# Kernel tuning notes

Measured on AMD Instinct MI355X. Metric: run time of the kernel, lower is better.

Reference implementation:

```python
import jax, jax.numpy as jnp
import numpy as np
from jax import lax

DIM = 64
E = int(DIM * 1.2)  # 76
E4 = E * 4          # 304
P = 8               # patch size
B, H, W = 2, 256, 256
THR = 1e-10


def setup_inputs() -> dict:
    key = jax.random.key(0)
    ks = jax.random.split(key, 5)
    x = jax.random.normal(ks[0], (B, DIM, H, W), dtype=jnp.float32)
    w_hidden = jax.random.normal(ks[1], (E4, DIM), dtype=jnp.float32) * 0.05
    w_dw = jax.random.normal(ks[2], (E4, 1, 3, 3), dtype=jnp.float32) * 0.2
    w_proj = jax.random.normal(ks[3], (DIM, 3 * E), dtype=jnp.float32) * 0.05
    fft_param = jnp.ones((E, 1, 1, P, P // 2 + 1), dtype=jnp.float32)
    ln1_w = jnp.ones((E,), jnp.float32); ln1_b = jnp.zeros((E,), jnp.float32)
    ln2_w = jnp.ones((E,), jnp.float32); ln2_b = jnp.zeros((E,), jnp.float32)
    ln3_w = jnp.ones((E,), jnp.float32); ln3_b = jnp.zeros((E,), jnp.float32)
    return dict(x=x, w_hidden=w_hidden, w_dw=w_dw, w_proj=w_proj,
                fft_param=fft_param, ln1_w=ln1_w, ln1_b=ln1_b,
                ln2_w=ln2_w, ln2_b=ln2_b, ln3_w=ln3_w, ln3_b=ln3_b)


def _replace_denormals(z, thr=THR):
    r, i = z.real, z.imag
    r = jnp.where((r < thr) & (r > -thr), thr, r)
    i = jnp.where((i < thr) & (i > -thr), thr, i)
    return lax.complex(r, i)


def _patch(t):  # b c H W -> b c h w P P
    b, c, h, w = t.shape
    return t.reshape(b, c, h // P, P, w // P, P).transpose(0, 1, 2, 4, 3, 5)


def _unpatch(t):  # b c h w P P -> b c H W
    b, c, h, w, p1, p2 = t.shape
    return t.transpose(0, 1, 2, 4, 3, 5).reshape(b, c, h * p1, w * p2)


def _layernorm(t, w, b):  # normalize over channel axis (axis=1), biased var
    mu = jnp.mean(t, axis=1, keepdims=True)
    var = jnp.mean((t - mu) ** 2, axis=1, keepdims=True)
    return (t - mu) / jnp.sqrt(var + 1e-5) * w[None, :, None, None] + b[None, :, None, None]


def reference(x, w_hidden, w_dw, w_proj, fft_param,
              ln1_w, ln1_b, ln2_w, ln2_b, ln3_w, ln3_b):
    hidden = jnp.einsum('bchw,oc->bohw', x, w_hidden)  # 1x1 conv
    hdw = lax.conv_general_dilated(
        hidden, w_dw, window_strides=(1, 1), padding='SAME',
        dimension_numbers=('NCHW', 'OIHW', 'NCHW'), feature_group_count=E4)
    q, k, v, v_value = jnp.split(hdw, 4, axis=1)

    qf = jnp.fft.rfft2(_patch(q))
    kf = jnp.fft.rfft2(_patch(k))
    vf = jnp.fft.rfft2(_patch(v)) * fft_param  # broadcast [E,1,1,P,P//2+1]
    vf = _replace_denormals(vf)

    qk = _replace_denormals(qf * kf)
    qka = jnp.abs(qk)
    v_a = jnp.abs(vf)
    v_p = jnp.arctan2(vf.imag, vf.real)

    qf = _replace_denormals(qf)
    kf = _replace_denormals(kf)
    qkp = jnp.arctan2(qf.imag, qf.real) - jnp.arctan2(kf.imag, kf.real)

    out1 = jnp.fft.irfft2(lax.complex(v_a * jnp.cos(qkp), v_a * jnp.sin(qkp)), s=(P, P))
    out2 = jnp.fft.irfft2(lax.complex(qka * jnp.cos(v_p), qka * jnp.sin(v_p)), s=(P, P))
    out3 = jnp.fft.irfft2(lax.complex(qka * jnp.cos(qkp), qka * jnp.sin(qkp)), s=(P, P))

    out1 = _layernorm(_unpatch(out1), ln1_w, ln1_b)
    out2 = _layernorm(_unpatch(out2), ln2_w, ln2_b)
    out3 = _layernorm(_unpatch(out3), ln3_w, ln3_b)

    cat = jnp.concatenate([v_value * out1, v_value * out2, v_value * out3], axis=1)
    return jnp.einsum('bchw,oc->bohw', cat, w_proj)
```

## Files before the change

### kernel.cpp

```cpp
#include <hip/hip_runtime.h>
#include <cstdint>
#include <cstddef>

constexpr int HWSZ = 65536;
constexpr size_t CH_ELEMS = (size_t)304 * HWSZ;
constexpr int WT_H_ELEMS = 64 * 304;
constexpr int WT_P_ELEMS = 228 * 64;

constexpr int TP = 261;
constexpr int GS = 10 * TP;

#define C1F 0.70710678118654752f
#define S2F 1.41421356237309505f

__device__ __forceinline__ float4 f4(float v) { return make_float4(v, v, v, v); }
__device__ __forceinline__ float4 operator+(float4 a, float4 b) { return make_float4(a.x+b.x, a.y+b.y, a.z+b.z, a.w+b.w); }
__device__ __forceinline__ float4 operator-(float4 a, float4 b) { return make_float4(a.x-b.x, a.y-b.y, a.z-b.z, a.w-b.w); }
__device__ __forceinline__ float4 operator*(float4 a, float4 b) { return make_float4(a.x*b.x, a.y*b.y, a.z*b.z, a.w*b.w); }
__device__ __forceinline__ float4& operator+=(float4& a, float4 b) { a.x+=b.x; a.y+=b.y; a.z+=b.z; a.w+=b.w; return a; }

__global__ __launch_bounds__(256) void k_prep(const float* __restrict__ wh,
                                              const float* __restrict__ wp,
                                              float* __restrict__ wt_h,
                                              float* __restrict__ wt_p) {
    int i = blockIdx.x * 256 + threadIdx.x;
    if (i < 64 * 304) {
        int o = i / 64, k = i % 64;
        wt_h[k * 304 + o] = wh[i];
    }
    int j = i - 64 * 304;
    if (j >= 0 && j < 64 * 228) {
        int o = j / 228, cc = j % 228;
        wt_p[cc * 64 + o] = wp[j];
    }
}

__global__ __launch_bounds__(256) void k_conv1(const float* __restrict__ xb,
                                               const float* __restrict__ wt,
                                               float* __restrict__ hidden) {
    int sp = blockIdx.x * 256 + threadIdx.x;
    int gbase = blockIdx.y * 38;
    float acc[38];
#pragma unroll
    for (int i = 0; i < 38; i++) acc[i] = 0.f;
#pragma unroll
    for (int kc = 0; kc < 64; kc += 16) {
        float xv[16];
#pragma unroll
        for (int k = 0; k < 16; k++) xv[k] = xb[(size_t)(kc + k) * HWSZ + sp];
#pragma unroll
        for (int k = 0; k < 16; k++) {
            const float* wrow = wt + (kc + k) * 304 + gbase;
#pragma unroll
            for (int i = 0; i < 38; i++) acc[i] = fmaf(xv[k], wrow[i], acc[i]);
        }
    }
#pragma unroll
    for (int i = 0; i < 38; i++) hidden[(size_t)(gbase + i) * HWSZ + sp] = acc[i];
}

__device__ __forceinline__ void rfft8(const float a[8], float Xr[5], float Xi[5]) {
    float u0 = a[0] + a[4], u1 = a[0] - a[4];
    float u2 = a[2] + a[6], u3 = a[2] - a[6];
    float u4 = a[1] + a[5], p  = a[1] - a[5];
    float u6 = a[3] + a[7], q  = a[3] - a[7];
    Xr[0] = u0 + u2 + u4 + u6;        Xi[0] = 0.f;
    Xr[1] = u1 + C1F * (p - q);       Xi[1] = -u3 - C1F * (p + q);
    Xr[2] = u0 - u2;                  Xi[2] = -(u4 - u6);
    Xr[3] = u1 - C1F * (p - q);       Xi[3] = u3 - C1F * (p + q);
    Xr[4] = u0 + u2 - u4 - u6;        Xi[4] = 0.f;
}

__device__ __forceinline__ void irfft8(const float Xr[5], const float Xi[5], float y[8]) {
    float A = Xr[0], B = Xr[4];
    float cr = Xr[1], ci = Xi[1], dr = Xr[2], di = Xi[2], er = Xr[3], ei = Xi[3];
    float abp = A + B, abm = A - B;
    float ccm = S2F * (cr - ci), ccp = S2F * (cr + ci);
    float eep = S2F * (er + ei), eem = S2F * (er - ei);
    float dr2 = 2.f * dr, di2 = 2.f * di;
    float cep = 2.f * (cr + er);
    float ci2 = 2.f * ci, ei2 = 2.f * ei;
    y[0] = abp + cep + dr2;
    y[1] = abm + ccm - di2 - eep;
    y[2] = abp - dr2 - ci2 + ei2;
    y[3] = abm - ccp + di2 + eem;
    y[4] = abp - cep + dr2;
    y[5] = abm - ccm - di2 + eep;
    y[6] = abp - dr2 + ci2 - ei2;
    y[7] = abm + ccp + di2 - eem;
}

__device__ __forceinline__ void bf_stage(float zr[15], float zi[15], int mask,
                                         float Ar, float Ai, float Br, float Bi) {
#pragma unroll
    for (int j = 0; j < 15; j++) {
        float or_ = __shfl_xor(zr[j], mask);
        float oi_ = __shfl_xor(zi[j], mask);
        float nr = Ar * zr[j] - Ai * zi[j] + Br * or_ - Bi * oi_;
        float ni = Ar * zi[j] + Ai * zr[j] + Br * oi_ + Bi * or_;
        zr[j] = nr; zi[j] = ni;
    }
}

__device__ __forceinline__ void cfwd15(float zr[15], float zi[15], int r) {
    int m = r & 3;
    float wr = (m == 0) ? 1.f : (m == 1) ? C1F : (m == 2) ? 0.f : -C1F;
    float wi = (m == 0) ? 0.f : (m == 1) ? -C1F : (m == 2) ? -1.f : -C1F;
    bool up = r >= 4;
    bf_stage(zr, zi, 4, up ? -wr : 1.f, up ? -wi : 0.f, up ? wr : 1.f, up ? wi : 0.f);
    bool u2 = (r & 2) != 0;
    float w2r = (r & 1) ? 0.f : 1.f, w2i = (r & 1) ? -1.f : 0.f;
    bf_stage(zr, zi, 2, u2 ? -w2r : 1.f, u2 ? -w2i : 0.f, u2 ? w2r : 1.f, u2 ? w2i : 0.f);
    bf_stage(zr, zi, 1, (r & 1) ? -1.f : 1.f, 0.f, 1.f, 0.f);
}

__device__ __forceinline__ void cinv15(float zr[15], float zi[15], int r) {
    bf_stage(zr, zi, 1, (r & 1) ? -1.f : 1.f, 0.f, 1.f, 0.f);
    float a2r, a2i, b2r, b2i;
    if ((r & 2) == 0) { a2r = 1.f; a2i = 0.f; b2r = (r & 1) ? 0.f : 1.f; b2i = (r & 1) ? 1.f : 0.f; }
    else             { a2r = (r & 1) ? 0.f : -1.f; a2i = (r & 1) ? -1.f : 0.f; b2r = 1.f; b2i = 0.f; }
    bf_stage(zr, zi, 2, a2r, a2i, b2r, b2i);
    int m = r & 3;
    float wr = (m == 0) ? 1.f : (m == 1) ? C1F : (m == 2) ? 0.f : -C1F;
    float wi = (m == 0) ? 0.f : (m == 1) ? C1F : (m == 2) ? 1.f : C1F;
    bool up = r >= 4;
    bf_stage(zr, zi, 4, up ? -wr : 1.f, up ? -wi : 0.f, up ? 1.f : wr, up ? 0.f : wi);
}

__global__ __launch_bounds__(256) void k_dwfft(const float* __restrict__ hidden,
                                               const float* __restrict__ wdw,
                                               float* __restrict__ hdwb,
                                               const float* __restrict__ fft_param) {
    int ph = blockIdx.x, c = blockIdx.y;
    int t = threadIdx.x;
    int p = t >> 3, r = t & 7;
    int br = ((r & 1) << 2) | (r & 2) | (r >> 2);
    int r0 = ph * 8;

    __shared__ float tile[4 * GS];

#pragma unroll
    for (int j = 0; j < 10; j++) {
        int idx = j * 256 + t;
        int g = idx / 640;
        int rem = idx - g * 640;
        int rr = rem >> 6, c4 = rem & 63;
        int gr = r0 - 1 + rr;
        float4 val = f4(0.f);
        if (gr >= 0 && gr < 256)
            val = *(const float4*)(hidden + (size_t)(g * 76 + c) * HWSZ + gr * 256 + c4 * 4);
        float* d = tile + g * GS + rr * TP + c4 * 4;
        d[0] = val.x; d[1] = val.y; d[2] = val.z; d[3] = val.w;
    }
    __syncthreads();

    float zr[15], zi[15];

    for (int g = 0; g < 3; g++) {
        float w[9];
#pragma unroll
        for (int i = 0; i < 9; i++) w[i] = wdw[(76 * g + c) * 9 + i];
        float acc[8];
#pragma unroll
        for (int j = 0; j < 8; j++) acc[j] = 0.f;
#pragma unroll
        for (int rr = 0; rr < 3; rr++) {
            float v[10];
            int base = g * GS + (r + rr) * TP + p * 8;
            v[0] = (p > 0) ? tile[base - 1] : 0.f;
#pragma unroll
            for (int j = 0; j < 8; j++) v[j + 1] = tile[base + j];
            v[9] = (p < 31) ? tile[base + 8] : 0.f;
#pragma unroll
            for (int j = 0; j < 8; j++)
                acc[j] += w[rr * 3 + 0] * v[j] + w[rr * 3 + 1] * v[j + 1] + w[rr * 3 + 2] * v[j + 2];
        }
        float Xr[5], Xi[5];
        rfft8(acc, Xr, Xi);
        int s0 = (g == 0) ? 0 : (g == 1) ? 5 : 10;
#pragma unroll
        for (int v = 0; v < 5; v++) { zr[s0 + v] = Xr[v]; zi[s0 + v] = Xi[v]; }
    }

    {
        float w[9];
#pragma unroll
        for (int i = 0; i < 9; i++) w[i] = wdw[(228 + c) * 9 + i];
        float cl[10], cm[10], cr_[10];
#pragma unroll
        for (int rr = 0; rr < 10; rr++) {
            int base = 3 * GS + rr * TP + t;
            cm[rr]  = tile[base];
            cl[rr]  = (t > 0)   ? tile[base - 1] : 0.f;
            cr_[rr] = (t < 255) ? tile[base + 1] : 0.f;
        }
        float* outp = hdwb + (size_t)(228 + c) * HWSZ + (size_t)r0 * 256 + t;
#pragma unroll
        for (int rr = 0; rr < 8; rr++) {
            float s = cl[rr] * w[0] + cm[rr] * w[1] + cr_[rr] * w[2]
                    + cl[rr + 1] * w[3] + cm[rr + 1] * w[4] + cr_[rr + 1] * w[5]
                    + cl[rr + 2] * w[6] + cm[rr + 2] * w[7] + cr_[rr + 2] * w[8];
            outp[(size_t)rr * 256] = s;
        }
    }

    cfwd15(zr, zi, r);

    const float inv64 = 0.015625f;
#pragma unroll
    for (int v = 0; v < 5; v++) {
        float pf = fft_param[(c * 8 + br) * 5 + v];
        float vr = zr[10 + v] * pf, vi = zi[10 + v] * pf;
        float qr = zr[v], qi = zi[v], kr = zr[5 + v], ki = zi[5 + v];
        float cr = qr * kr + qi * ki;
        float ci = qi * kr - qr * ki;
        float m2q = cr * cr + ci * ci, m2v = vr * vr + vi * vi;
        float rq = rsqrtf(fmaxf(m2q, 1e-38f));
        float rv = rsqrtf(fmaxf(m2v, 1e-38f));
        float s  = sqrtf(m2v) * rq * inv64;
        float tt = sqrtf(m2q) * rv * inv64;
        zr[v] = cr * s;           zi[v] = ci * s;
        zr[10 + v] = vr * tt;     zi[10 + v] = vi * tt;
        zr[5 + v] = cr * inv64;   zi[5 + v] = ci * inv64;
    }

    cinv15(zr, zi, r);

    size_t obase = (size_t)c * HWSZ + (size_t)(r0 + r) * 256 + p * 8;
    float Xr[5], Xi[5], y[8];
#pragma unroll
    for (int v = 0; v < 5; v++) { Xr[v] = zr[v]; Xi[v] = zi[v]; }
    irfft8(Xr, Xi, y);
    { float4 f0 = {y[0],y[1],y[2],y[3]}, f1 = {y[4],y[5],y[6],y[7]};
      *(float4*)(hdwb + obase) = f0; *(float4*)(hdwb + obase + 4) = f1; }
#pragma unroll
    for (int v = 0; v < 5; v++) { Xr[v] = zr[10 + v]; Xi[v] = zi[10 + v]; }
    irfft8(Xr, Xi, y);
    { float4 f0 = {y[0],y[1],y[2],y[3]}, f1 = {y[4],y[5],y[6],y[7]};
      *(float4*)(hdwb + obase + (size_t)76 * HWSZ) = f0;
      *(float4*)(hdwb + obase + (size_t)76 * HWSZ + 4) = f1; }
#pragma unroll
    for (int v = 0; v < 5; v++) { Xr[v] = zr[5 + v]; Xi[v] = zi[5 + v]; }
    irfft8(Xr, Xi, y);
    { float4 f0 = {y[0],y[1],y[2],y[3]}, f1 = {y[4],y[5],y[6],y[7]};
      *(float4*)(hdwb + obase + (size_t)152 * HWSZ) = f0;
      *(float4*)(hdwb + obase + (size_t)152 * HWSZ + 4) = f1; }
}

__global__ __launch_bounds__(512) void k_outb(const float* __restrict__ hdwb,
                                              const float* __restrict__ wt_p,
                                              const float* __restrict__ ln1w, const float* __restrict__ ln1b,
                                              const float* __restrict__ ln2w, const float* __restrict__ ln2b,
                                              const float* __restrict__ ln3w, const float* __restrict__ ln3b,
                                              float* __restrict__ outb) {
    int lane = threadIdx.x & 63;
    int w = threadIdx.x >> 6;
    int px = blockIdx.x * 256 + lane * 4;
    const float* hb = hdwb + px;

    float4 s1 = f4(0), q1 = f4(0), s2 = f4(0), q2 = f4(0), s3 = f4(0), q3 = f4(0);
    for (int c = w; c < 76; c += 8) {
        float4 v1 = *(const float4*)(hb + (size_t)c * HWSZ);
        float4 v2 = *(const float4*)(hb + (size_t)(76 + c) * HWSZ);
        float4 v3 = *(const float4*)(hb + (size_t)(152 + c) * HWSZ);
        s1 += v1; q1 += v1 * v1;
        s2 += v2; q2 += v2 * v2;
        s3 += v3; q3 += v3 * v3;
    }
    __shared__ float4 sred[6][8][64];
    sred[0][w][lane] = s1; sred[1][w][lane] = q1;
    sred[2][w][lane] = s2; sred[3][w][lane] = q2;
    sred[4][w][lane] = s3; sred[5][w][lane] = q3;
    __syncthreads();
    s1 = f4(0); q1 = f4(0); s2 = f4(0); q2 = f4(0); s3 = f4(0); q3 = f4(0);
#pragma unroll
    for (int k = 0; k < 8; k++) {
        s1 += sred[0][k][lane]; q1 += sred[1][k][lane];
        s2 += sred[2][k][lane]; q2 += sred[3][k][lane];
        s3 += sred[4][k][lane]; q3 += sred[5][k][lane];
    }

    const float4 invE = f4(1.f / 76.f);
    float4 m1 = s1 * invE, m2 = s2 * invE, m3 = s3 * invE;
    float4 vr1 = q1 * invE - m1 * m1, vr2 = q2 * invE - m2 * m2, vr3 = q3 * invE - m3 * m3;
    float4 r1, r2, r3;
    r1.x = rsqrtf(fmaxf(vr1.x, 0.f) + 1e-5f); r1.y = rsqrtf(fmaxf(vr1.y, 0.f) + 1e-5f);
    r1.z = rsqrtf(fmaxf(vr1.z, 0.f) + 1e-5f); r1.w = rsqrtf(fmaxf(vr1.w, 0.f) + 1e-5f);
    r2.x = rsqrtf(fmaxf(vr2.x, 0.f) + 1e-5f); r2.y = rsqrtf(fmaxf(vr2.y, 0.f) + 1e-5f);
    r2.z = rsqrtf(fmaxf(vr2.z, 0.f) + 1e-5f); r2.w = rsqrtf(fmaxf(vr2.w, 0.f) + 1e-5f);
    r3.x = rsqrtf(fmaxf(vr3.x, 0.f) + 1e-5f); r3.y = rsqrtf(fmaxf(vr3.y, 0.f) + 1e-5f);
    r3.z = rsqrtf(fmaxf(vr3.z, 0.f) + 1e-5f); r3.w = rsqrtf(fmaxf(vr3.w, 0.f) + 1e-5f);

    int o0 = w * 8;
    float4 acc[8];
#pragma unroll
    for (int i = 0; i < 8; i++) acc[i] = f4(0);

    float4 pv = *(const float4*)(hb + (size_t)228 * HWSZ);
    float4 p1 = *(const float4*)(hb);
    float4 p2 = *(const float4*)(hb + (size_t)76 * HWSZ);
    float4 p3 = *(const float4*)(hb + (size_t)152 * HWSZ);
    for (int c = 0; c < 76; c++) {
        float4 vv = pv, l1 = p1, l2 = p2, l3 = p3;
        if (c < 75) {
            pv = *(const float4*)(hb + (size_t)(229 + c) * HWSZ);
            p1 = *(const float4*)(hb + (size_t)(1 + c) * HWSZ);
            p2 = *(const float4*)(hb + (size_t)(77 + c) * HWSZ);
            p3 = *(const float4*)(hb + (size_t)(153 + c) * HWSZ);
        }
        float4 v1 = ((l1 - m1) * r1 * f4(ln1w[c]) + f4(ln1b[c])) * vv;
        float4 v2 = ((l2 - m2) * r2 * f4(ln2w[c]) + f4(ln2b[c])) * vv;
        float4 v3 = ((l3 - m3) * r3 * f4(ln3w[c]) + f4(ln3b[c])) * vv;
        const float* w1 = wt_p + c * 64 + o0;
        const float* w2 = wt_p + (76 + c) * 64 + o0;
        const float* w3 = wt_p + (152 + c) * 64 + o0;
#pragma unroll
        for (int i = 0; i < 8; i++)
            acc[i] += v1 * f4(w1[i]) + v2 * f4(w2[i]) + v3 * f4(w3[i]);
    }
#pragma unroll
    for (int i = 0; i < 8; i++)
        *(float4*)(outb + (size_t)(o0 + i) * HWSZ + px) = acc[i];
}

extern "C" void kernel_launch(void* const* d_in, const int* in_sizes, int n_in,
                              void* d_out, int out_size, void* d_ws, size_t ws_size,
                              hipStream_t stream) {
    const float* x    = (const float*)d_in[0];
    const float* wh   = (const float*)d_in[1];
    const float* wdw  = (const float*)d_in[2];
    const float* wp   = (const float*)d_in[3];
    const float* fftp = (const float*)d_in[4];
    const float* ln1w = (const float*)d_in[5];
    const float* ln1b = (const float*)d_in[6];
    const float* ln2w = (const float*)d_in[7];
    const float* ln2b = (const float*)d_in[8];
    const float* ln3w = (const float*)d_in[9];
    const float* ln3b = (const float*)d_in[10];
    float* out = (float*)d_out;
    float* ws  = (float*)d_ws;

    const size_t wbytes = (size_t)(WT_H_ELEMS + WT_P_ELEMS) * 4;
    const size_t need = 2 * CH_ELEMS * 4 + wbytes;
    if (ws_size < need) return;

    float* hidden = ws;
    float* hdwb   = ws + CH_ELEMS;
    float* wt_h   = ws + 2 * CH_ELEMS;
    float* wt_p   = wt_h + WT_H_ELEMS;

    hipLaunchKernelGGL(k_prep, dim3(134), dim3(256), 0, stream, wh, wp, wt_h, wt_p);

    for (int b = 0; b < 2; b++) {
        const float* xb = x + (size_t)b * 64 * HWSZ;
        hipLaunchKernelGGL(k_conv1, dim3(256, 8), dim3(256), 0, stream, xb, wt_h, hidden);
        hipLaunchKernelGGL(k_dwfft, dim3(32, 76), dim3(256), 0, stream, hidden, wdw, hdwb, fftp);
        hipLaunchKernelGGL(k_outb, dim3(256), dim3(512), 0, stream, hdwb, wt_p,
                           ln1w, ln1b, ln2w, ln2b, ln3w, ln3b,
                           out + (size_t)b * 64 * HWSZ);
    }
}
```

Measured before the change: 469.1 us.

## Batch both images in one output kernel, widen conv1 channel tile, double-buffer loads

k_conv1 now computes 76 output channels per thread instead of 38 and loads input in chunks of 8, halving grid.y so each input element is reread fewer times. When the workspace is large enough, both batch elements keep their own hdwb buffer and a single k_outb launch with grid.y=2 covers both images, doubling the parallelism of the output stage and dropping one launch. The k_outb channel loop is unrolled by two with two independent prefetch buffers to hide more load latency. The wider conv1 accumulator array raises register pressure and may cut occupancy or cause spills, and the batched path needs an extra channel-sized workspace buffer.

```diff
diff --git a/kernel.cpp b/kernel.cpp
--- a/kernel.cpp
+++ b/kernel.cpp
@@ -39,24 +39,24 @@
                                                const float* __restrict__ wt,
                                                float* __restrict__ hidden) {
     int sp = blockIdx.x * 256 + threadIdx.x;
-    int gbase = blockIdx.y * 38;
-    float acc[38];
-#pragma unroll
-    for (int i = 0; i < 38; i++) acc[i] = 0.f;
-#pragma unroll
-    for (int kc = 0; kc < 64; kc += 16) {
-        float xv[16];
-#pragma unroll
-        for (int k = 0; k < 16; k++) xv[k] = xb[(size_t)(kc + k) * HWSZ + sp];
-#pragma unroll
-        for (int k = 0; k < 16; k++) {
+    int gbase = blockIdx.y * 76;
+    float acc[76];
+#pragma unroll
+    for (int i = 0; i < 76; i++) acc[i] = 0.f;
+#pragma unroll
+    for (int kc = 0; kc < 64; kc += 8) {
+        float xv[8];
+#pragma unroll
+        for (int k = 0; k < 8; k++) xv[k] = xb[(size_t)(kc + k) * HWSZ + sp];
+#pragma unroll
+        for (int k = 0; k < 8; k++) {
             const float* wrow = wt + (kc + k) * 304 + gbase;
 #pragma unroll
-            for (int i = 0; i < 38; i++) acc[i] = fmaf(xv[k], wrow[i], acc[i]);
-        }
-    }
-#pragma unroll
-    for (int i = 0; i < 38; i++) hidden[(size_t)(gbase + i) * HWSZ + sp] = acc[i];
+            for (int i = 0; i < 76; i++) acc[i] = fmaf(xv[k], wrow[i], acc[i]);
+        }
+    }
+#pragma unroll
+    for (int i = 0; i < 76; i++) hidden[(size_t)(gbase + i) * HWSZ + sp] = acc[i];
 }
 
 __device__ __forceinline__ void rfft8(const float a[8], float Xr[5], float Xi[5]) {
@@ -247,16 +247,17 @@
       *(float4*)(hdwb + obase + (size_t)152 * HWSZ + 4) = f1; }
 }
 
-__global__ __launch_bounds__(512) void k_outb(const float* __restrict__ hdwb,
+__global__ __launch_bounds__(512) void k_outb(const float* __restrict__ hdwb, size_t bstride,
                                               const float* __restrict__ wt_p,
                                               const float* __restrict__ ln1w, const float* __restrict__ ln1b,
                                               const float* __restrict__ ln2w, const float* __restrict__ ln2b,
                                               const float* __restrict__ ln3w, const float* __restrict__ ln3b,
-                                              float* __restrict__ outb) {
+                                              float* __restrict__ outb, size_t obstride) {
     int lane = threadIdx.x & 63;
     int w = threadIdx.x >> 6;
     int px = blockIdx.x * 256 + lane * 4;
-    const float* hb = hdwb + px;
+    const float* hb = hdwb + (size_t)blockIdx.y * bstride + px;
+    float* ob = outb + (size_t)blockIdx.y * obstride + px;
 
     float4 s1 = f4(0), q1 = f4(0), s2 = f4(0), q2 = f4(0), s3 = f4(0), q3 = f4(0);
     for (int c = w; c < 76; c += 8) {
@@ -296,31 +297,42 @@
 #pragma unroll
     for (int i = 0; i < 8; i++) acc[i] = f4(0);
 
-    float4 pv = *(const float4*)(hb + (size_t)228 * HWSZ);
-    float4 p1 = *(const float4*)(hb);
-    float4 p2 = *(const float4*)(hb + (size_t)76 * HWSZ);
-    float4 p3 = *(const float4*)(hb + (size_t)152 * HWSZ);
-    for (int c = 0; c < 76; c++) {
-        float4 vv = pv, l1 = p1, l2 = p2, l3 = p3;
-        if (c < 75) {
-            pv = *(const float4*)(hb + (size_t)(229 + c) * HWSZ);
-            p1 = *(const float4*)(hb + (size_t)(1 + c) * HWSZ);
-            p2 = *(const float4*)(hb + (size_t)(77 + c) * HWSZ);
-            p3 = *(const float4*)(hb + (size_t)(153 + c) * HWSZ);
-        }
-        float4 v1 = ((l1 - m1) * r1 * f4(ln1w[c]) + f4(ln1b[c])) * vv;
-        float4 v2 = ((l2 - m2) * r2 * f4(ln2w[c]) + f4(ln2b[c])) * vv;
-        float4 v3 = ((l3 - m3) * r3 * f4(ln3w[c]) + f4(ln3b[c])) * vv;
-        const float* w1 = wt_p + c * 64 + o0;
-        const float* w2 = wt_p + (76 + c) * 64 + o0;
-        const float* w3 = wt_p + (152 + c) * 64 + o0;
-#pragma unroll
-        for (int i = 0; i < 8; i++)
-            acc[i] += v1 * f4(w1[i]) + v2 * f4(w2[i]) + v3 * f4(w3[i]);
-    }
+#define LD(cc, off) (*(const float4*)(hb + (size_t)((off) + (cc)) * HWSZ))
+    float4 av = LD(0, 228), a1 = LD(0, 0), a2 = LD(0, 76), a3 = LD(0, 152);
+    float4 bv = LD(1, 228), b1 = LD(1, 0), b2 = LD(1, 76), b3 = LD(1, 152);
+    for (int c = 0; c < 76; c += 2) {
+        {
+            float4 vv = av, l1 = a1, l2 = a2, l3 = a3;
+            if (c + 2 < 76) { av = LD(c + 2, 228); a1 = LD(c + 2, 0); a2 = LD(c + 2, 76); a3 = LD(c + 2, 152); }
+            float4 v1 = ((l1 - m1) * r1 * f4(ln1w[c]) + f4(ln1b[c])) * vv;
+            float4 v2 = ((l2 - m2) * r2 * f4(ln2w[c]) + f4(ln2b[c])) * vv;
+            float4 v3 = ((l3 - m3) * r3 * f4(ln3w[c]) + f4(ln3b[c])) * vv;
+            const float* w1 = wt_p + c * 64 + o0;
+            const float* w2 = wt_p + (76 + c) * 64 + o0;
+            const float* w3 = wt_p + (152 + c) * 64 + o0;
+#pragma unroll
+            for (int i = 0; i < 8; i++)
+                acc[i] += v1 * f4(w1[i]) + v2 * f4(w2[i]) + v3 * f4(w3[i]);
+        }
+        {
+            int cc = c + 1;
+            float4 vv = bv, l1 = b1, l2 = b2, l3 = b3;
+            if (c + 3 < 76) { bv = LD(c + 3, 228); b1 = LD(c + 3, 0); b2 = LD(c + 3, 76); b3 = LD(c + 3, 152); }
+            float4 v1 = ((l1 - m1) * r1 * f4(ln1w[cc]) + f4(ln1b[cc])) * vv;
+            float4 v2 = ((l2 - m2) * r2 * f4(ln2w[cc]) + f4(ln2b[cc])) * vv;
+            float4 v3 = ((l3 - m3) * r3 * f4(ln3w[cc]) + f4(ln3b[cc])) * vv;
+            const float* w1 = wt_p + cc * 64 + o0;
+            const float* w2 = wt_p + (76 + cc) * 64 + o0;
+            const float* w3 = wt_p + (152 + cc) * 64 + o0;
+#pragma unroll
+            for (int i = 0; i < 8; i++)
+                acc[i] += v1 * f4(w1[i]) + v2 * f4(w2[i]) + v3 * f4(w3[i]);
+        }
+    }
+#undef LD
 #pragma unroll
     for (int i = 0; i < 8; i++)
-        *(float4*)(outb + (size_t)(o0 + i) * HWSZ + px) = acc[i];
+        *(float4*)(ob + (size_t)(o0 + i) * HWSZ) = acc[i];
 }
 
 extern "C" void kernel_launch(void* const* d_in, const int* in_sizes, int n_in,
@@ -341,22 +353,47 @@
     float* ws  = (float*)d_ws;
 
     const size_t wbytes = (size_t)(WT_H_ELEMS + WT_P_ELEMS) * 4;
-    const size_t need = 2 * CH_ELEMS * 4 + wbytes;
-    if (ws_size < need) return;
-
-    float* hidden = ws;
-    float* hdwb   = ws + CH_ELEMS;
-    float* wt_h   = ws + 2 * CH_ELEMS;
-    float* wt_p   = wt_h + WT_H_ELEMS;
+    const size_t need1 = 2 * CH_ELEMS * 4 + wbytes;
+    const size_t need2 = 3 * CH_ELEMS * 4 + wbytes;
+    if (ws_size < need1) return;
+    bool dual = (ws_size >= need2);
+
+    float* hdwb0, *hdwb1, *hidden, *wt_h, *wt_p;
+    if (dual) {
+        hdwb0  = ws;
+        hdwb1  = ws + CH_ELEMS;
+        hidden = ws + 2 * CH_ELEMS;
+        wt_h   = ws + 3 * CH_ELEMS;
+    } else {
+        hdwb0  = ws;
+        hdwb1  = ws;
+        hidden = ws + CH_ELEMS;
+        wt_h   = ws + 2 * CH_ELEMS;
+    }
+    wt_p = wt_h + WT_H_ELEMS;
 
     hipLaunchKernelGGL(k_prep, dim3(134), dim3(256), 0, stream, wh, wp, wt_h, wt_p);
 
-    for (int b = 0; b < 2; b++) {
-        const float* xb = x + (size_t)b * 64 * HWSZ;
-        hipLaunchKernelGGL(k_conv1, dim3(256, 8), dim3(256), 0, stream, xb, wt_h, hidden);
-        hipLaunchKernelGGL(k_dwfft, dim3(32, 76), dim3(256), 0, stream, hidden, wdw, hdwb, fftp);
-        hipLaunchKernelGGL(k_outb, dim3(256), dim3(512), 0, stream, hdwb, wt_p,
+    if (dual) {
+        for (int b = 0; b < 2; b++) {
+            const float* xb = x + (size_t)b * 64 * HWSZ;
+            float* hdwb = b ? hdwb1 : hdwb0;
+            hipLaunchKernelGGL(k_conv1, dim3(256, 4), dim3(256), 0, stream, xb, wt_h, hidden);
+            hipLaunchKernelGGL(k_dwfft, dim3(32, 76), dim3(256), 0, stream, hidden, wdw, hdwb, fftp);
+        }
+        hipLaunchKernelGGL(k_outb, dim3(256, 2), dim3(512), 0, stream,
+                           hdwb0, CH_ELEMS, wt_p,
                            ln1w, ln1b, ln2w, ln2b, ln3w, ln3b,
-                           out + (size_t)b * 64 * HWSZ);
-    }
-}
+                           out, (size_t)64 * HWSZ);
+    } else {
+        for (int b = 0; b < 2; b++) {
+            const float* xb = x + (size_t)b * 64 * HWSZ;
+            hipLaunchKernelGGL(k_conv1, dim3(256, 4), dim3(256), 0, stream, xb, wt_h, hidden);
+            hipLaunchKernelGGL(k_dwfft, dim3(32, 76), dim3(256), 0, stream, hidden, wdw, hdwb0, fftp);
+            hipLaunchKernelGGL(k_outb, dim3(256, 1), dim3(512), 0, stream,
+                               hdwb0, (size_t)0, wt_p,
+                               ln1w, ln1b, ln2w, ln2b, ln3w, ln3b,
+                               out + (size_t)b * 64 * HWSZ, (size_t)0);
+        }
+    }
+}
```

After: 517.2 us. 1.1x slower.
